# Kernel optimization log

Measured on AMD Instinct MI355X. Metric: run time of the kernel, lower is better.

The kernel has to match this reference:

```python
import jax, jax.numpy as jnp
import numpy as np

B = 8
C_IN = 3
DIV = 7
N0 = 20 * 4 ** DIV      # 327680 pixels at division 7
N1 = N0 // 4            # 81920 pixels at division 6
N2 = N1 // 4            # 20480 pixels at division 5
K_CONV = 10             # SpherePHD conv kernel size (triangle + 9 neighbors)
K_ADJ = 4               # pooling neighborhood (pixel + 3 edge-adjacent)


def setup_inputs() -> dict:
    key = jax.random.key(0)
    ks = jax.random.split(key, 15)
    x = jax.random.normal(ks[0], (B, C_IN, N0), dtype=jnp.float32)
    conv_t0 = jax.random.randint(ks[1], (N0, K_CONV), 0, N0, dtype=jnp.int32)
    conv_t1 = jax.random.randint(ks[2], (N1, K_CONV), 0, N1, dtype=jnp.int32)
    conv_t2 = jax.random.randint(ks[3], (N2, K_CONV), 0, N2, dtype=jnp.int32)
    adj0 = jax.random.randint(ks[4], (N0, K_ADJ), 0, N0, dtype=jnp.int32)
    adj1 = jax.random.randint(ks[5], (N1, K_ADJ), 0, N1, dtype=jnp.int32)
    pool0 = jax.random.randint(ks[6], (N1,), 0, N0, dtype=jnp.int32)
    pool1 = jax.random.randint(ks[7], (N2,), 0, N1, dtype=jnp.int32)
    w1 = jax.random.normal(ks[8], (16, C_IN, K_CONV), dtype=jnp.float32) * 0.1
    b1 = jax.random.normal(ks[9], (16,), dtype=jnp.float32) * 0.1
    w2 = jax.random.normal(ks[10], (32, 16, K_CONV), dtype=jnp.float32) * 0.1
    b2 = jax.random.normal(ks[11], (32,), dtype=jnp.float32) * 0.1
    w3 = jax.random.normal(ks[12], (10, 32, K_CONV), dtype=jnp.float32) * 0.1
    b3 = jax.random.normal(ks[13], (10,), dtype=jnp.float32) * 0.1
    return {"x": x, "conv_t0": conv_t0, "conv_t1": conv_t1, "conv_t2": conv_t2,
            "adj0": adj0, "adj1": adj1, "pool0": pool0, "pool1": pool1,
            "w1": w1, "b1": b1, "w2": w2, "b2": b2, "w3": w3, "b3": b3}


def phd_conv2d(x, table, w, b):
    # x: [B, Cin, N]; table: [N, K] neighbor indices; w: [Cout, Cin, K]
    g = x[:, :, table]                               # gather -> [B, Cin, N, K]
    return jnp.einsum('bcnk,ock->bon', g, w) + b[None, :, None]


def phd_maxpool(x, adj, pool):
    # max over adjacency neighborhood, then 4:1 downsample via pooling table
    m = jnp.max(x[:, :, adj], axis=-1)               # [B, C, N_fine]
    return m[:, :, pool]                             # [B, C, N_coarse]


def reference(x, conv_t0, conv_t1, conv_t2, adj0, adj1, pool0, pool1,
              w1, b1, w2, b2, w3, b3):
    h = phd_conv2d(x, conv_t0, w1, b1)               # [B, 16, N0]
    h = phd_maxpool(h, adj0, pool0)                  # [B, 16, N1]
    h = phd_conv2d(h, conv_t1, w2, b2)               # [B, 32, N1]
    h = phd_maxpool(h, adj1, pool1)                  # [B, 32, N2]
    h = phd_conv2d(h, conv_t2, w3, b3)               # [B, 10, N2]
    return jnp.mean(h, axis=-1)                      # PHD_avgpool -> [B, 10]
```

## Files before the change

kernel.cpp:

```cpp
#include <hip/hip_runtime.h>

#define NB 8
#define CIN 3
#define N0 327680
#define N1 81920
#define N2 20480
#define KC 10
#define KA 4

typedef __attribute__((ext_vector_type(8))) short bf16x8;
typedef __attribute__((ext_vector_type(4))) float f32x4;
typedef int4  __attribute__((aligned(4))) int4_u;

__device__ __forceinline__ unsigned f2bf(float f) {
  unsigned u = __float_as_uint(f);
  return (u + 0x7FFFu + ((u >> 16) & 1u)) >> 16;
}

union bfrag { bf16x8 v; unsigned u[4]; };

__global__ __launch_bounds__(256) void kpre(
    const float* __restrict__ x, uint4* __restrict__ xT64,
    const int* __restrict__ conv_t0, const int* __restrict__ conv_t1,
    const int* __restrict__ conv_t2,
    const int* __restrict__ adj0, const int* __restrict__ adj1,
    const int* __restrict__ pool0, const int* __restrict__ pool1,
    int* __restrict__ fidxM, int* __restrict__ fidxP, float* __restrict__ A12,
    const float* __restrict__ w1, const float* __restrict__ w2,
    const float* __restrict__ w3, const float* __restrict__ b3,
    unsigned short* __restrict__ wB1, unsigned short* __restrict__ wB,
    float* __restrict__ w3t, float* __restrict__ out) {
  int blk = blockIdx.x;
  if (blk < 1280) {
    int n = blk * 256 + threadIdx.x;
    unsigned d[12];
#pragma unroll
    for (int bp = 0; bp < 4; ++bp) {
      const float* pe = x + (size_t)(2 * bp) * CIN * N0 + n;
      const float* po = pe + (size_t)CIN * N0;
      float e0 = pe[0], e1 = pe[N0], e2 = pe[2 * N0];
      float o0 = po[0], o1 = po[N0], o2 = po[2 * N0];
      d[bp * 3 + 0] = f2bf(e0) | (f2bf(e1) << 16);
      d[bp * 3 + 1] = f2bf(e2) | (f2bf(o0) << 16);
      d[bp * 3 + 2] = f2bf(o1) | (f2bf(o2) << 16);
    }
    uint4* dst = xT64 + (size_t)n * 4;
    dst[0] = make_uint4(d[0], d[1], d[2], d[3]);
    dst[1] = make_uint4(d[4], d[5], d[6], d[7]);
    dst[2] = make_uint4(d[8], d[9], d[10], d[11]);
    dst[3] = make_uint4(0, 0, 0, 0);
  } else if (blk < 2560) {
    int t = (blk - 1280) * 256 + threadIdx.x;
    int j = t >> 2, p = t & 3;
    int pj = pool0[j];
    int pos = adj0[pj * KA + p];
    const int2* s0 = (const int2*)(conv_t0 + (size_t)pos * 10);
    int2 q0 = s0[0], q1 = s0[1], q2 = s0[2], q3 = s0[3], q4 = s0[4];
    int4_u* dM = (int4_u*)(fidxM + (size_t)t * 12);
    dM[0] = make_int4(q0.x * 64, q0.y * 64, q4.x * 64, q4.y * 64);
    dM[1] = make_int4(q1.x * 64, q1.y * 64, q2.x * 64, q2.y * 64);
    dM[2] = make_int4(q3.x * 64, q3.y * 64, 0, 0);
    if (j < N2) {
      int qj = pool1[j];
      int qos = adj1[qj * KA + p];
      const int2* s1 = (const int2*)(conv_t1 + (size_t)qos * 10);
      int2 r0 = s1[0], r1 = s1[1], r2 = s1[2], r3 = s1[3], r4 = s1[4];
      int4_u* dP = (int4_u*)(fidxP + (size_t)t * 12);
      dP[0] = make_int4(r0.x * 32, r1.x * 32, r2.x * 32, r3.x * 32);
      dP[1] = make_int4(r4.x * 32, 0,          r0.y * 32, r1.y * 32);
      dP[2] = make_int4(r2.y * 32, r3.y * 32, r4.y * 32, 0);
    }
  } else if (blk < 3360) {
    int t = (blk - 2560) * 256 + threadIdx.x;
    int n = conv_t2[t];
    int k = t % 10;
    atomicAdd(&A12[n * 12 + k], 1.0f);
  } else {
    int t = (blk - 3360) * 256 + threadIdx.x;
    if (t < 1024) {
      int ch = t >> 9, rest = t & 511, l = rest >> 3, e = rest & 7;
      int k = ch * 32 + ((l >> 4) * 8) + e;
      int tap = k >> 2, cc = k & 3;
      float v = (tap < KC && cc < CIN) ? w1[((l & 15) * CIN + cc) * KC + tap] : 0.f;
      wB1[t] = (unsigned short)f2bf(v);
    }
    if (t < 5120) {
      int e = t & 7, l = (t >> 3) & 63, nt = (t >> 9) & 1, q = t >> 10;
      int kc = q * 32 + ((l >> 4) * 8) + e;
      int tap = kc >> 4, c = kc & 15;
      int o = nt * 16 + (l & 15);
      wB[t] = (unsigned short)f2bf(w2[(o * 16 + c) * KC + tap]);
    }
    if (t < 3200) { int o = t % 10, r = t / 10, c = r & 31, k = r >> 5;
                    w3t[t] = w3[(o * 32 + c) * KC + k]; }
    if (t < 80)   out[t] = b3[t % 10];
  }
}

#define TR0(s) ((s) == 0 ? Ra.x : (s) == 1 ? Ra.w : (s) == 2 ? Rb.z : Rc.y)
#define TR1(s) ((s) == 0 ? Ra.y : (s) == 1 ? Rb.x : (s) == 2 ? Rb.w : Rc.z)
#define TR2(s) ((s) == 0 ? Ra.z : (s) == 1 ? Rb.y : (s) == 2 ? Rc.x : Rc.w)

__global__ __launch_bounds__(256, 4) void k1(
    const char* __restrict__ xT64, const int* __restrict__ fidxM,
    const bf16x8* __restrict__ wB1, const float* __restrict__ b1,
    unsigned short* __restrict__ h2) {
  int blk = blockIdx.x;
  int wave = threadIdx.x >> 6;
  int lane = threadIdx.x & 63;
  int col = lane & 15, hi = lane >> 4;
  int tile = blk * 4 + wave;
  bf16x8 B0 = wB1[lane];
  bf16x8 B1 = wB1[64 + lane];
  float bias = b1[col];
  int seloff = ((hi + 1) >> 1) << 2;

  int4 I = *(const int4_u*)(fidxM + ((size_t)tile * 16 + col) * 12 + seloff);
  int a0 = (hi == 2) ? I.z : I.x;
  int a1 = (hi == 2) ? I.w : I.y;
  const uint4* r0p = (const uint4*)(xT64 + a0);
  const uint4* r1p = (const uint4*)(xT64 + a1);
  uint4 R0a = r0p[0], R0b = r0p[1], R0c = r0p[2];
  uint4 R1a = r1p[0], R1b = r1p[1], R1c = r1p[2];
  uint4 zz = make_uint4(0, 0, 0, 0);
  uint4 R2a = zz, R2b = zz, R2c = zz, R3a = zz, R3b = zz, R3c = zz;
  if (hi == 0) {
    const uint4* r2p = (const uint4*)(xT64 + I.z);
    const uint4* r3p = (const uint4*)(xT64 + I.w);
    R2a = r2p[0]; R2b = r2p[1]; R2c = r2p[2];
    R3a = r3p[0]; R3b = r3p[1]; R3c = r3p[2];
  }
  size_t j = (size_t)tile * 4 + hi;
  unsigned short* dst = h2 + j * 16 + col;

#define DO_BPAIR(s)                                                           \
  {                                                                           \
    unsigned t0, t1, t2, u0, u1, u2, v0, v1, v2, w0, w1, w2;                  \
    { uint4 Ra = R0a, Rb = R0b, Rc = R0c;                                     \
      t0 = TR0(s); t1 = TR1(s); t2 = TR2(s); }                                \
    { uint4 Ra = R1a, Rb = R1b, Rc = R1c;                                     \
      u0 = TR0(s); u1 = TR1(s); u2 = TR2(s); }                                \
    { uint4 Ra = R2a, Rb = R2b, Rc = R2c;                                     \
      v0 = TR0(s); v1 = TR1(s); v2 = TR2(s); }                                \
    { uint4 Ra = R3a, Rb = R3b, Rc = R3c;                                     \
      w0 = TR0(s); w1 = TR1(s); w2 = TR2(s); }                                \
    bfrag A0c0, A1c0, A0c1, A1c1;                                             \
    A0c0.u[0] = t0; A0c0.u[1] = t1 & 0xFFFFu;                                 \
    A0c0.u[2] = u0; A0c0.u[3] = u1 & 0xFFFFu;                                 \
    A1c0.u[0] = (t1 >> 16) | (t2 << 16); A1c0.u[1] = t2 >> 16;                \
    A1c0.u[2] = (u1 >> 16) | (u2 << 16); A1c0.u[3] = u2 >> 16;                \
    A0c1.u[0] = v0; A0c1.u[1] = v1 & 0xFFFFu;                                 \
    A0c1.u[2] = w0; A0c1.u[3] = w1 & 0xFFFFu;                                 \
    A1c1.u[0] = (v1 >> 16) | (v2 << 16); A1c1.u[1] = v2 >> 16;                \
    A1c1.u[2] = (w1 >> 16) | (w2 << 16); A1c1.u[3] = w2 >> 16;                \
    f32x4 z = {0.f, 0.f, 0.f, 0.f};                                           \
    f32x4 acc0 = __builtin_amdgcn_mfma_f32_16x16x32_bf16(A0c0.v, B0, z, 0, 0, 0); \
    acc0 = __builtin_amdgcn_mfma_f32_16x16x32_bf16(A0c1.v, B1, acc0, 0, 0, 0);    \
    f32x4 acc1 = __builtin_amdgcn_mfma_f32_16x16x32_bf16(A1c0.v, B0, z, 0, 0, 0); \
    acc1 = __builtin_amdgcn_mfma_f32_16x16x32_bf16(A1c1.v, B1, acc1, 0, 0, 0);    \
    float m0 = fmaxf(fmaxf(acc0[0], acc0[1]), fmaxf(acc0[2], acc0[3])) + bias;    \
    float m1 = fmaxf(fmaxf(acc1[0], acc1[1]), fmaxf(acc1[2], acc1[3])) + bias;    \
    dst[(size_t)(2 * (s)) * N1 * 16]     = (unsigned short)f2bf(m0);          \
    dst[(size_t)(2 * (s) + 1) * N1 * 16] = (unsigned short)f2bf(m1);          \
  }
  DO_BPAIR(0)
  DO_BPAIR(1)
  DO_BPAIR(2)
  DO_BPAIR(3)
#undef DO_BPAIR
}

__global__ __launch_bounds__(256, 4) void k2(
    const char* __restrict__ h2, const int* __restrict__ fidxP,
    const float* __restrict__ A12, const bf16x8* __restrict__ wB,
    const float* __restrict__ b2, float* __restrict__ G) {
  __shared__ float GL[320];
  int blk = blockIdx.x;
  int b = blk & 7;
  int wave = threadIdx.x >> 6;
  int lane = threadIdx.x & 63;
  int col = lane & 15;
  int odd = (lane >> 5) & 1;
  int tile0 = ((blk >> 3) * 4 + wave) * 8;
  const char* hb = h2 + (size_t)b * N1 * 32 + ((lane >> 4) & 1) * 16;
  for (int i = threadIdx.x; i < 320; i += 256) GL[i] = 0.f;
  __syncthreads();

  bf16x8 Bf[10];
#pragma unroll
  for (int i = 0; i < 10; ++i) Bf[i] = wB[i * 64 + lane];
  float bias0 = b2[col];
  float bias1 = b2[16 + col];
  float g0[10], g1[10];
#pragma unroll
  for (int k = 0; k < 10; ++k) { g0[k] = 0.f; g1[k] = 0.f; }

#pragma unroll 2
  for (int i = 0; i < 8; ++i) {
    int tile = tile0 + i;
    const int* fp = fidxP + ((size_t)tile * 16 + col) * 12 + odd * 6;
    int4 T = *(const int4_u*)fp;
    int  T4 = fp[4];
    f32x4 acc0 = {0.f, 0.f, 0.f, 0.f};
    f32x4 acc1 = {0.f, 0.f, 0.f, 0.f};
    bf16x8 A;
    A = *(const bf16x8*)(hb + T.x);
    acc0 = __builtin_amdgcn_mfma_f32_16x16x32_bf16(A, Bf[0], acc0, 0, 0, 0);
    acc1 = __builtin_amdgcn_mfma_f32_16x16x32_bf16(A, Bf[1], acc1, 0, 0, 0);
    A = *(const bf16x8*)(hb + T.y);
    acc0 = __builtin_amdgcn_mfma_f32_16x16x32_bf16(A, Bf[2], acc0, 0, 0, 0);
    acc1 = __builtin_amdgcn_mfma_f32_16x16x32_bf16(A, Bf[3], acc1, 0, 0, 0);
    A = *(const bf16x8*)(hb + T.z);
    acc0 = __builtin_amdgcn_mfma_f32_16x16x32_bf16(A, Bf[4], acc0, 0, 0, 0);
    acc1 = __builtin_amdgcn_mfma_f32_16x16x32_bf16(A, Bf[5], acc1, 0, 0, 0);
    A = *(const bf16x8*)(hb + T.w);
    acc0 = __builtin_amdgcn_mfma_f32_16x16x32_bf16(A, Bf[6], acc0, 0, 0, 0);
    acc1 = __builtin_amdgcn_mfma_f32_16x16x32_bf16(A, Bf[7], acc1, 0, 0, 0);
    A = *(const bf16x8*)(hb + T4);
    acc0 = __builtin_amdgcn_mfma_f32_16x16x32_bf16(A, Bf[8], acc0, 0, 0, 0);
    acc1 = __builtin_amdgcn_mfma_f32_16x16x32_bf16(A, Bf[9], acc1, 0, 0, 0);
    float m0 = fmaxf(fmaxf(acc0[0], acc0[1]), fmaxf(acc0[2], acc0[3])) + bias0;
    float m1 = fmaxf(fmaxf(acc1[0], acc1[1]), fmaxf(acc1[2], acc1[3])) + bias1;
    int j = tile * 4 + (lane >> 4);
    const float* ar = A12 + (size_t)j * 12;
    float4 a0 = *(const float4*)ar;
    float4 a1 = *(const float4*)(ar + 4);
    float2 a2 = *(const float2*)(ar + 8);
    float av[10] = {a0.x, a0.y, a0.z, a0.w, a1.x, a1.y, a1.z, a1.w, a2.x, a2.y};
#pragma unroll
    for (int k = 0; k < 10; ++k) {
      g0[k] = fmaf(m0, av[k], g0[k]);
      g1[k] = fmaf(m1, av[k], g1[k]);
    }
  }
#pragma unroll
  for (int k = 0; k < 10; ++k) {
    g0[k] += __shfl_xor(g0[k], 16); g0[k] += __shfl_xor(g0[k], 32);
    g1[k] += __shfl_xor(g1[k], 16); g1[k] += __shfl_xor(g1[k], 32);
  }
  if (lane < 16) {
#pragma unroll
    for (int k = 0; k < 10; ++k) {
      atomicAdd(&GL[col * 10 + k], g0[k]);
      atomicAdd(&GL[(col + 16) * 10 + k], g1[k]);
    }
  }
  __syncthreads();
  for (int i = threadIdx.x; i < 320; i += 256)
    atomicAdd(&G[b * 320 + i], GL[i]);
}

__global__ __launch_bounds__(256) void k3c(
    const float* __restrict__ G, const float* __restrict__ w3t,
    float* __restrict__ out) {
  int t = blockIdx.x * 256 + threadIdx.x;
  int pair = t >> 5, c = t & 31;
  int b = pair / 10, o = pair % 10;
  float s = 0.f;
#pragma unroll
  for (int k = 0; k < KC; ++k)
    s += G[b * 320 + c * 10 + k] * w3t[k * 320 + c * 10 + o];
#pragma unroll
  for (int off = 1; off < 32; off <<= 1) s += __shfl_xor(s, off);
  if ((threadIdx.x & 31) == 0) atomicAdd(&out[pair], s * (1.0f / N2));
}

extern "C" void kernel_launch(void* const* d_in, const int* in_sizes, int n_in,
                              void* d_out, int out_size, void* d_ws, size_t ws_size,
                              hipStream_t stream) {
  const float* x       = (const float*)d_in[0];
  const int*   conv_t0 = (const int*)d_in[1];
  const int*   conv_t1 = (const int*)d_in[2];
  const int*   conv_t2 = (const int*)d_in[3];
  const int*   adj0    = (const int*)d_in[4];
  const int*   adj1    = (const int*)d_in[5];
  const int*   pool0   = (const int*)d_in[6];
  const int*   pool1   = (const int*)d_in[7];
  const float* w1      = (const float*)d_in[8];
  const float* b1      = (const float*)d_in[9];
  const float* w2      = (const float*)d_in[10];
  const float* b2      = (const float*)d_in[11];
  const float* w3      = (const float*)d_in[12];
  const float* b3      = (const float*)d_in[13];
  float* out  = (float*)d_out;
  float* wsf  = (float*)d_ws;

  uint4* xT64  = (uint4*)wsf;
  unsigned short* h2b = (unsigned short*)(wsf + 5242880);
  int* fidxM   = (int*)(wsf + 2 * 5242880);
  int* fidxP   = fidxM + (size_t)N1 * 4 * 12;
  float* A12   = (float*)(fidxP + (size_t)N2 * 4 * 12);
  float* G     = A12 + (size_t)N2 * 12;
  unsigned short* wB1 = (unsigned short*)(G + 2560);
  unsigned short* wB  = wB1 + 1024;
  float* w3t   = (float*)(wB + 5120);

  hipMemsetAsync(A12, 0, (size_t)(N2 * 12 + 2560) * 4, stream);
  kpre<<<3380, 256, 0, stream>>>(x, xT64, conv_t0, conv_t1, conv_t2,
                                 adj0, adj1, pool0, pool1,
                                 fidxM, fidxP, A12,
                                 w1, w2, w3, b3, wB1, wB, w3t, out);
  k1<<<5120, 256, 0, stream>>>((const char*)xT64, fidxM, (const bf16x8*)wB1, b1, h2b);
  k2<<<1280, 256, 0, stream>>>((const char*)h2b, fidxP, A12, (const bf16x8*)wB, b2, G);
  k3c<<<10, 256, 0, stream>>>(G, w3t, out);
}
```

Before: 131.9 us.

## Split preprocessing kernel and move layer-2 setup after first conv

The single preprocessing kernel is split into two. kpreA handles the input transpose, now four pixels per thread with float4 loads, plus the layer-1 index table, zeroing of the count and accumulator buffers (replacing a separate memset call), and the layer-1 weights. kpreB builds the layer-2 index table, the conv_t2 tap counts and the remaining weights, and is launched between k1 and k2. The aim is to cut one launch, vectorise the transpose loads, and shorten the critical path before k1. The price is an extra kernel boundary between k1 and k2 on the same stream.

```diff
diff --git a/kernel.cpp b/kernel.cpp
--- a/kernel.cpp
+++ b/kernel.cpp
@@ -19,38 +19,46 @@
 
 union bfrag { bf16x8 v; unsigned u[4]; };
 
-__global__ __launch_bounds__(256) void kpre(
+__global__ __launch_bounds__(256) void kpreA(
     const float* __restrict__ x, uint4* __restrict__ xT64,
-    const int* __restrict__ conv_t0, const int* __restrict__ conv_t1,
-    const int* __restrict__ conv_t2,
-    const int* __restrict__ adj0, const int* __restrict__ adj1,
-    const int* __restrict__ pool0, const int* __restrict__ pool1,
-    int* __restrict__ fidxM, int* __restrict__ fidxP, float* __restrict__ A12,
-    const float* __restrict__ w1, const float* __restrict__ w2,
-    const float* __restrict__ w3, const float* __restrict__ b3,
-    unsigned short* __restrict__ wB1, unsigned short* __restrict__ wB,
-    float* __restrict__ w3t, float* __restrict__ out) {
+    const int* __restrict__ conv_t0, const int* __restrict__ adj0,
+    const int* __restrict__ pool0, int* __restrict__ fidxM,
+    float* __restrict__ A12G, const float* __restrict__ w1,
+    unsigned short* __restrict__ wB1) {
   int blk = blockIdx.x;
-  if (blk < 1280) {
-    int n = blk * 256 + threadIdx.x;
-    unsigned d[12];
+  if (blk < 320) {
+    int t = blk * 256 + threadIdx.x;
+    int n = t * 4;
+    unsigned d[4][12];
 #pragma unroll
     for (int bp = 0; bp < 4; ++bp) {
       const float* pe = x + (size_t)(2 * bp) * CIN * N0 + n;
       const float* po = pe + (size_t)CIN * N0;
-      float e0 = pe[0], e1 = pe[N0], e2 = pe[2 * N0];
-      float o0 = po[0], o1 = po[N0], o2 = po[2 * N0];
-      d[bp * 3 + 0] = f2bf(e0) | (f2bf(e1) << 16);
-      d[bp * 3 + 1] = f2bf(e2) | (f2bf(o0) << 16);
-      d[bp * 3 + 2] = f2bf(o1) | (f2bf(o2) << 16);
-    }
-    uint4* dst = xT64 + (size_t)n * 4;
-    dst[0] = make_uint4(d[0], d[1], d[2], d[3]);
-    dst[1] = make_uint4(d[4], d[5], d[6], d[7]);
-    dst[2] = make_uint4(d[8], d[9], d[10], d[11]);
-    dst[3] = make_uint4(0, 0, 0, 0);
-  } else if (blk < 2560) {
-    int t = (blk - 1280) * 256 + threadIdx.x;
+      float4 e0 = *(const float4*)(pe);
+      float4 e1 = *(const float4*)(pe + N0);
+      float4 e2 = *(const float4*)(pe + 2 * N0);
+      float4 o0 = *(const float4*)(po);
+      float4 o1 = *(const float4*)(po + N0);
+      float4 o2 = *(const float4*)(po + 2 * N0);
+      const float* E0 = &e0.x; const float* E1 = &e1.x; const float* E2 = &e2.x;
+      const float* O0 = &o0.x; const float* O1 = &o1.x; const float* O2 = &o2.x;
+#pragma unroll
+      for (int r = 0; r < 4; ++r) {
+        d[r][bp * 3 + 0] = f2bf(E0[r]) | (f2bf(E1[r]) << 16);
+        d[r][bp * 3 + 1] = f2bf(E2[r]) | (f2bf(O0[r]) << 16);
+        d[r][bp * 3 + 2] = f2bf(O1[r]) | (f2bf(O2[r]) << 16);
+      }
+    }
+#pragma unroll
+    for (int r = 0; r < 4; ++r) {
+      uint4* dst = xT64 + (size_t)(n + r) * 4;
+      dst[0] = make_uint4(d[r][0], d[r][1], d[r][2],  d[r][3]);
+      dst[1] = make_uint4(d[r][4], d[r][5], d[r][6],  d[r][7]);
+      dst[2] = make_uint4(d[r][8], d[r][9], d[r][10], d[r][11]);
+      dst[3] = make_uint4(0, 0, 0, 0);
+    }
+  } else if (blk < 1600) {
+    int t = (blk - 320) * 256 + threadIdx.x;
     int j = t >> 2, p = t & 3;
     int pj = pool0[j];
     int pos = adj0[pj * KA + p];
@@ -60,23 +68,11 @@
     dM[0] = make_int4(q0.x * 64, q0.y * 64, q4.x * 64, q4.y * 64);
     dM[1] = make_int4(q1.x * 64, q1.y * 64, q2.x * 64, q2.y * 64);
     dM[2] = make_int4(q3.x * 64, q3.y * 64, 0, 0);
-    if (j < N2) {
-      int qj = pool1[j];
-      int qos = adj1[qj * KA + p];
-      const int2* s1 = (const int2*)(conv_t1 + (size_t)qos * 10);
-      int2 r0 = s1[0], r1 = s1[1], r2 = s1[2], r3 = s1[3], r4 = s1[4];
-      int4_u* dP = (int4_u*)(fidxP + (size_t)t * 12);
-      dP[0] = make_int4(r0.x * 32, r1.x * 32, r2.x * 32, r3.x * 32);
-      dP[1] = make_int4(r4.x * 32, 0,          r0.y * 32, r1.y * 32);
-      dP[2] = make_int4(r2.y * 32, r3.y * 32, r4.y * 32, 0);
-    }
-  } else if (blk < 3360) {
-    int t = (blk - 2560) * 256 + threadIdx.x;
-    int n = conv_t2[t];
-    int k = t % 10;
-    atomicAdd(&A12[n * 12 + k], 1.0f);
+  } else if (blk < 1843) {
+    int t = (blk - 1600) * 256 + threadIdx.x;
+    if (t < 62080) ((float4*)A12G)[t] = make_float4(0.f, 0.f, 0.f, 0.f);
   } else {
-    int t = (blk - 3360) * 256 + threadIdx.x;
+    int t = (blk - 1843) * 256 + threadIdx.x;
     if (t < 1024) {
       int ch = t >> 9, rest = t & 511, l = rest >> 3, e = rest & 7;
       int k = ch * 32 + ((l >> 4) * 8) + e;
@@ -84,6 +80,35 @@
       float v = (tap < KC && cc < CIN) ? w1[((l & 15) * CIN + cc) * KC + tap] : 0.f;
       wB1[t] = (unsigned short)f2bf(v);
     }
+  }
+}
+
+__global__ __launch_bounds__(256) void kpreB(
+    const int* __restrict__ conv_t1, const int* __restrict__ conv_t2,
+    const int* __restrict__ adj1, const int* __restrict__ pool1,
+    int* __restrict__ fidxP, float* __restrict__ A12,
+    const float* __restrict__ w2, const float* __restrict__ w3,
+    const float* __restrict__ b3, unsigned short* __restrict__ wB,
+    float* __restrict__ w3t, float* __restrict__ out) {
+  int blk = blockIdx.x;
+  if (blk < 320) {
+    int t = blk * 256 + threadIdx.x;
+    int j = t >> 2, p = t & 3;
+    int qj = pool1[j];
+    int qos = adj1[qj * KA + p];
+    const int2* s1 = (const int2*)(conv_t1 + (size_t)qos * 10);
+    int2 r0 = s1[0], r1 = s1[1], r2 = s1[2], r3 = s1[3], r4 = s1[4];
+    int4_u* dP = (int4_u*)(fidxP + (size_t)t * 12);
+    dP[0] = make_int4(r0.x * 32, r1.x * 32, r2.x * 32, r3.x * 32);
+    dP[1] = make_int4(r4.x * 32, 0,          r0.y * 32, r1.y * 32);
+    dP[2] = make_int4(r2.y * 32, r3.y * 32, r4.y * 32, 0);
+  } else if (blk < 1120) {
+    int t = (blk - 320) * 256 + threadIdx.x;
+    int n = conv_t2[t];
+    int k = t % 10;
+    atomicAdd(&A12[n * 12 + k], 1.0f);
+  } else {
+    int t = (blk - 1120) * 256 + threadIdx.x;
     if (t < 5120) {
       int e = t & 7, l = (t >> 3) & 63, nt = (t >> 9) & 1, q = t >> 10;
       int kc = q * 32 + ((l >> 4) * 8) + e;
@@ -295,12 +320,11 @@
   unsigned short* wB  = wB1 + 1024;
   float* w3t   = (float*)(wB + 5120);
 
-  hipMemsetAsync(A12, 0, (size_t)(N2 * 12 + 2560) * 4, stream);
-  kpre<<<3380, 256, 0, stream>>>(x, xT64, conv_t0, conv_t1, conv_t2,
-                                 adj0, adj1, pool0, pool1,
-                                 fidxM, fidxP, A12,
-                                 w1, w2, w3, b3, wB1, wB, w3t, out);
+  kpreA<<<1847, 256, 0, stream>>>(x, xT64, conv_t0, adj0, pool0, fidxM,
+                                  A12, w1, wB1);
   k1<<<5120, 256, 0, stream>>>((const char*)xT64, fidxM, (const bf16x8*)wB1, b1, h2b);
+  kpreB<<<1140, 256, 0, stream>>>(conv_t1, conv_t2, adj1, pool1, fidxP, A12,
+                                  w2, w3, b3, wB, w3t, out);
   k2<<<1280, 256, 0, stream>>>((const char*)h2b, fidxP, A12, (const bf16x8*)wB, b2, G);
   k3c<<<10, 256, 0, stream>>>(G, w3t, out);
 }
```

Measured after the change: 139.1 us. 1.05x slower.
